# Optimization experiments

Hardware: AMD Instinct MI355X
Metric: run time of the kernel (lower is better)

## Reference

```python
import jax, jax.numpy as jnp
import numpy as np
import math

SQRT2 = float(np.sqrt(2.0))
INV_SQRT_2PI = float(1.0 / np.sqrt(2.0 * np.pi))


def _trunc_prob(x, mu, sigma):
    # Faithful port of TruncNormal.prob with a=-10, b=10
    a, b = -10.0, 10.0
    phi_b = 0.5 * (1.0 + jax.scipy.special.erf((b - mu) / sigma / SQRT2))
    phi_a = 0.5 * (1.0 + jax.scipy.special.erf((a - mu) / sigma / SQRT2))
    xs = jnp.where(x > b, x + 100.0, x)
    xs = jnp.where(xs < a, xs - 100.0, xs)
    xn = (xs - mu) / sigma
    dens = jnp.exp(-0.5 * xn * xn) * INV_SQRT_2PI
    dens = jnp.where((xn > b) | (xn < a), 0.0, dens)
    return dens / (phi_b - phi_a) + 1e-10


def _S_single(zg, tt, Wx, bx, Wt, bt, Wt2, bt2, Wf, bf, Wo, bo):
    # One tiny MLP applied to one group-slice zg (shape [g]) at scalar time tt.
    g = Wx.shape[0]
    x = jnp.tanh(Wx @ zg + bx)
    half = g // 2
    freqs = jnp.exp(jnp.arange(half, dtype=zg.dtype) * (-math.log(10000.0) / half))
    te = tt * freqs
    temb = jnp.concatenate([jnp.sin(te), jnp.cos(te)])  # [g]
    tv = jax.nn.gelu(Wt @ temb + bt, approximate=False)  # torch nn.GELU (exact)
    tv = Wt2 @ tv + bt2
    h = jnp.tanh(Wf @ (x + tv) + bf)
    return jnp.tanh(Wo @ h + bo)[0]  # scalar S


def _derivs(zg, tt, Wx, bx, Wt, bt, Wt2, bt2, Wf, bf, Wo, bo):
    p = (Wx, bx, Wt, bt, Wt2, bt2, Wf, bf, Wo, bo)
    f = lambda z_, t_: _S_single(z_, t_, *p)
    S = f(zg, tt)
    s_z = jax.grad(f, 0)(zg, tt)                    # dS/dz         [g]
    H = jax.jacfwd(jax.grad(f, 0), 0)(zg, tt)       # H[j,k]=d2S/dzj dzk  [g,g]
    dSdt = jax.grad(f, 1)(zg, tt)                   # dS/dt scalar
    return S, s_z, H, dSdt


def reference(z, time_step, mu, sigma, Wx, bx, Wt, bt, Wt2, bt2, Wf, bf, Wo, bo, beta):
    G, g = Wx.shape[0], Wx.shape[1]
    B = z.shape[0]
    tt = time_step[0]

    sig2 = sigma ** 2 + 1e-5
    nlp = -(z - mu) / sig2                                   # nabla_log_phi [B,n_in]
    dlp = -1.0 / sig2                                        # delta_log_phi (scalar-ish)
    dpp = ((z - mu) ** 2 - sigma ** 2) / (sigma ** 4 + 1e-5)  # delta_phi_over_phi
    rho = _trunc_prob(z, mu, sigma)

    to_g = lambda a: a.reshape(B, G, g).transpose(1, 0, 2)   # [G,B,g]
    zr, nlp_r, dpp_r, rho_r = to_g(z), to_g(nlp), to_g(dpp), to_g(rho)

    over_b = jax.vmap(_derivs, in_axes=(0, None) + (None,) * 10)
    over_g = jax.vmap(over_b, in_axes=(0, None) + (0,) * 10)
    S, s_z, H, dSdt = over_g(zr, tt, Wx, bx, Wt, bt, Wt2, bt2, Wf, bf, Wo, bo)
    # S [G,B], s_z [G,B,g], H [G,B,g,g], dSdt [G,B]

    bb = beta.reshape(G, 1, 1)
    u = S[..., None] - bb * jnp.log(jnp.prod(rho_r, axis=2, keepdims=True))  # [G,B,1]
    u_z = s_z - bb * nlp_r                                                    # [G,B,g]
    # torch grad(S.sum(), t): t is a single shared (1,1) tensor -> gradient sums over batch
    dSdt_sum = dSdt.sum(axis=1).reshape(G, 1, 1)
    # grad((rho*u_z).sum(), z_temp): rho and nabla_log_phi are constants wrt z_temp,
    # so gradient = sum_j rho_j * H[j,k]
    corr = jnp.einsum('gbj,gbjk->gbk', rho_r, H)
    u_t = dSdt_sum + bb * corr / (rho_r + 1e-5)
    # grad(s_z.sum(), z_temp)[k] = sum_j H[j,k]
    u_zz = H.sum(axis=2) - bb * dlp
    pde = u_t + 0.5 * u_z ** 2 + 0.125 * bb ** 2 * (nlp_r ** 2 - 2.0 * dpp_r)

    to_bn = lambda a: a.transpose(1, 0, 2).reshape(B, -1)
    return to_bn(pde), to_bn(u_z), u[:, :, 0].transpose(1, 0), to_bn(u_zz)


def setup_inputs() -> dict:
    B, N_IN, g = 8192, 512, 4
    G = N_IN // g
    key = jax.random.key(0)
    ks = jax.random.split(key, 16)

    def lin_w(k, fo, fi):
        return (jax.random.normal(k, (G, fo, fi), jnp.float32) / np.sqrt(fi)).astype(jnp.float32)

    def lin_b(k, fo):
        return (0.01 * jax.random.normal(k, (G, fo), jnp.float32)).astype(jnp.float32)

    return {
        "z": jax.random.normal(ks[0], (B, N_IN), jnp.float32),
        "time_step": jnp.ones((1,), jnp.float32),
        "mu": jnp.zeros((1,), jnp.float32),
        "sigma": jnp.ones((1,), jnp.float32),
        "Wx": lin_w(ks[1], g, g), "bx": lin_b(ks[2], g),
        "Wt": lin_w(ks[3], g, g), "bt": lin_b(ks[4], g),
        "Wt2": lin_w(ks[5], g, g), "bt2": lin_b(ks[6], g),
        "Wf": lin_w(ks[7], g, g), "bf": lin_b(ks[8], g),
        "Wo": lin_w(ks[9], 1, g), "bo": lin_b(ks[10], 1),
        "beta": jnp.ones((G, 1), jnp.float32),
    }
```

## Files before the change

### kernel.cpp

```cpp
#include <hip/hip_runtime.h>
#include <math.h>

#define NG 128
#define NIN 512
#define OFF1 4194304
#define OFF2 8388608
#define OFF3 9437184

#define INV_SQRT_2PI 0.3989422804014327f
#define INV_SQRT2    0.7071067811865476f

__device__ __forceinline__ float ftanh(float x){
    float e = __expf(2.0f*x);
    float r = __builtin_amdgcn_rcpf(e + 1.0f);
    return 1.0f - 2.0f*r;
}
__device__ __forceinline__ float frcp(float x){ return __builtin_amdgcn_rcpf(x); }

__device__ __forceinline__ float gelu_f(float x){
    return 0.5f*x*(1.0f + erff(x*INV_SQRT2));
}
__device__ __forceinline__ float gelu_df(float x){
    return 0.5f*(1.0f + erff(x*INV_SQRT2)) + x*INV_SQRT_2PI*__expf(-0.5f*x*x);
}

__global__ __launch_bounds__(256) void k_fused(const float* __restrict__ z,
    const float* __restrict__ ts,
    const float* __restrict__ mup, const float* __restrict__ sigp,
    const float* __restrict__ Wx, const float* __restrict__ bx,
    const float* __restrict__ Wt, const float* __restrict__ bt,
    const float* __restrict__ Wt2, const float* __restrict__ bt2,
    const float* __restrict__ Wf, const float* __restrict__ bf,
    const float* __restrict__ Wo, const float* __restrict__ bo,
    const float* __restrict__ betap,
    float* __restrict__ partial, float* __restrict__ out){
    const int tid  = threadIdx.x;
    const int gidx = tid & 127;
    const int lb   = tid >> 7;

    const float mu = mup[0], sigma = sigp[0];
    const float sig2     = sigma*sigma + 1e-5f;
    const float inv_sig2 = frcp(sig2);
    const float dlp      = -inv_sig2;
    const float inv_s4   = frcp(sigma*sigma*sigma*sigma + 1e-5f);
    const float inv_sig  = frcp(sigma);
    const float phi_b    = 0.5f*(1.0f+erff((10.0f-mu)*inv_sig*INV_SQRT2));
    const float phi_a    = 0.5f*(1.0f+erff((-10.0f-mu)*inv_sig*INV_SQRT2));
    const float invZ     = frcp(phi_b-phi_a);

    float wx[16], wf[16];
    #pragma unroll
    for (int i=0;i<4;i++){
        float4 a4 = ((const float4*)(Wx + gidx*16))[i];
        wx[i*4+0]=a4.x; wx[i*4+1]=a4.y; wx[i*4+2]=a4.z; wx[i*4+3]=a4.w;
        float4 b4 = ((const float4*)(Wf + gidx*16))[i];
        wf[i*4+0]=b4.x; wf[i*4+1]=b4.y; wf[i*4+2]=b4.z; wf[i*4+3]=b4.w;
    }
    float4 t4;
    t4 = ((const float4*)bx)[gidx];    float bxA[4]={t4.x,t4.y,t4.z,t4.w};
    t4 = ((const float4*)bf)[gidx];    float bfA[4]={t4.x,t4.y,t4.z,t4.w};
    t4 = ((const float4*)Wo)[gidx];    float w3[4] ={t4.x,t4.y,t4.z,t4.w};
    const float bo0 = bo[gidx];
    const float bb  = betap[gidx];

    float tvA[4], dtvA[4];
    {
        const float t  = ts[0];
        const float f1 = 0.01f;
        float te0 = t, te1 = t*f1;
        float s0, c0, s1, c1;
        __sincosf(te0, &s0, &c0);
        __sincosf(te1, &s1, &c1);
        float temb[4]  = { s0, s1, c0, c1 };
        float dtemb[4] = { c0, f1*c1, -s0, -f1*s1 };
        float tg[4], dg[4];
        #pragma unroll
        for (int i=0;i<4;i++){
            float a = bt[gidx*4+i], d = 0.0f;
            #pragma unroll
            for (int j=0;j<4;j++){
                float w = Wt[gidx*16+i*4+j];
                a += w*temb[j]; d += w*dtemb[j];
            }
            tg[i] = gelu_f(a);
            dg[i] = gelu_df(a)*d;
        }
        #pragma unroll
        for (int j=0;j<4;j++){
            float a = bt2[gidx*4+j], d = 0.0f;
            #pragma unroll
            for (int i=0;i<4;i++){
                float w = Wt2[gidx*16+j*4+i];
                a += w*tg[i]; d += w*dg[i];
            }
            tvA[j]  = a;
            dtvA[j] = d;
        }
    }

    float dsdt_acc = 0.0f;
    const int b_base = blockIdx.x*4 + lb*2;

    for (int r=0;r<2;r++){
        const int b = b_base + r;
        float4 zv = *((const float4*)(z + b*NIN + gidx*4));
        float zz[4]={zv.x,zv.y,zv.z,zv.w};

        float x[4], xp[4], u1[4];
        #pragma unroll
        for (int i=0;i<4;i++){
            float a = bxA[i] + wx[i*4]*zz[0]+wx[i*4+1]*zz[1]+wx[i*4+2]*zz[2]+wx[i*4+3]*zz[3];
            x[i] = ftanh(a); xp[i] = 1.0f - x[i]*x[i];
            u1[i] = x[i] + tvA[i];
        }
        float h[4], hp[4];
        float a3 = bo0;
        #pragma unroll
        for (int i=0;i<4;i++){
            float a = bfA[i] + wf[i*4]*u1[0]+wf[i*4+1]*u1[1]+wf[i*4+2]*u1[2]+wf[i*4+3]*u1[3];
            h[i] = ftanh(a); hp[i] = 1.0f - h[i]*h[i];
            a3 += w3[i]*h[i];
        }
        float S = ftanh(a3), sp = 1.0f - S*S;

        float Bm[16];
        #pragma unroll
        for (int i=0;i<4;i++){
            #pragma unroll
            for (int n=0;n<4;n++){
                float s = 0.0f;
                #pragma unroll
                for (int k=0;k<4;k++) s += wf[i*4+k]*xp[k]*wx[k*4+n];
                Bm[i*4+n]=s;
            }
        }
        float w3hp[4], v[4];
        #pragma unroll
        for (int i=0;i<4;i++){ w3hp[i]=w3[i]*hp[i]; v[i]=sp*w3hp[i]; }
        float q[4]={0.f,0.f,0.f,0.f};
        #pragma unroll
        for (int i=0;i<4;i++){
            #pragma unroll
            for (int j=0;j<4;j++) q[j] += v[i]*wf[i*4+j];
        }
        dsdt_acc += q[0]*dtvA[0]+q[1]*dtvA[1]+q[2]*dtvA[2]+q[3]*dtvA[3];

        float c[4];
        #pragma unroll
        for (int n=0;n<4;n++){
            float s=0.0f;
            #pragma unroll
            for (int i=0;i<4;i++) s += w3hp[i]*Bm[i*4+n];
            c[n]=s;
        }
        const float alpha = -2.0f*S*sp;
        float bet[4], gam[4];
        #pragma unroll
        for (int i=0;i<4;i++){ bet[i] = -2.0f*h[i]*v[i]; gam[i] = -2.0f*x[i]*xp[i]*q[i]; }

        float rho[4], nlp[4], dpp[4];
        #pragma unroll
        for (int j=0;j<4;j++){
            float zj = zz[j];
            float xs = zj > 10.0f ? zj+100.0f : zj;
            xs = xs < -10.0f ? xs-100.0f : xs;
            float xn = (xs-mu)*inv_sig;
            float dens = __expf(-0.5f*xn*xn)*INV_SQRT_2PI;
            dens = (xn > 10.0f || xn < -10.0f) ? 0.0f : dens;
            rho[j] = dens*invZ + 1e-10f;
            nlp[j] = -(zj-mu)*inv_sig2;
            float d = zj-mu;
            dpp[j] = (d*d - sigma*sigma)*inv_s4;
        }
        float u_val = S - bb*__logf(rho[0]*rho[1]*rho[2]*rho[3]);

        float rc=0.0f, scs=0.0f;
        #pragma unroll
        for (int j=0;j<4;j++){ rc += rho[j]*c[j]; scs += c[j]; }
        float rB[4], sB[4], rA[4], sA[4];
        #pragma unroll
        for (int i=0;i<4;i++){
            float r1=0.0f, s=0.0f, r2=0.0f, s2=0.0f;
            #pragma unroll
            for (int j=0;j<4;j++){
                r1 += rho[j]*Bm[i*4+j]; s  += Bm[i*4+j];
                r2 += rho[j]*wx[i*4+j]; s2 += wx[i*4+j];
            }
            rB[i]=r1; sB[i]=s; rA[i]=r2; sA[i]=s2;
        }

        float pde[4], uz[4], uzz[4];
        #pragma unroll
        for (int k=0;k<4;k++){
            float corr = alpha*rc*c[k];
            float hsum = alpha*scs*c[k];
            #pragma unroll
            for (int i=0;i<4;i++){
                corr += bet[i]*rB[i]*Bm[i*4+k];
                hsum += bet[i]*sB[i]*Bm[i*4+k];
                corr += gam[i]*rA[i]*wx[i*4+k];
                hsum += gam[i]*sA[i]*wx[i*4+k];
            }
            float uzk = sp*c[k] - bb*nlp[k];
            uz[k]  = uzk;
            uzz[k] = hsum - bb*dlp;
            pde[k] = bb*corr*frcp(rho[k]+1e-5f)
                   + 0.5f*uzk*uzk + 0.125f*bb*bb*(nlp[k]*nlp[k] - 2.0f*dpp[k]);
        }

        const int base = b*NIN + gidx*4;
        *((float4*)(out + base))        = make_float4(pde[0],pde[1],pde[2],pde[3]);
        *((float4*)(out + OFF1 + base)) = make_float4(uz[0],uz[1],uz[2],uz[3]);
        out[OFF2 + b*NG + gidx] = u_val;
        *((float4*)(out + OFF3 + base)) = make_float4(uzz[0],uzz[1],uzz[2],uzz[3]);
    }

    __shared__ float sred[256];
    sred[tid] = dsdt_acc;
    __syncthreads();
    if (tid < 128) partial[blockIdx.x*128 + tid] = sred[tid] + sred[tid+128];
}

__global__ __launch_bounds__(256) void k_red(const float* __restrict__ partial,
                                             float* __restrict__ dsum){
    int g = blockIdx.x;
    int tid = threadIdx.x;
    float a = 0.0f;
    for (int i=tid;i<2048;i+=256) a += partial[i*128+g];
    __shared__ float s[256];
    s[tid] = a;
    __syncthreads();
    if (tid < 64){
        a = s[tid] + s[tid+64] + s[tid+128] + s[tid+192];
        #pragma unroll
        for (int o=32;o>0;o>>=1) a += __shfl_down(a, o);
        if (tid==0) dsum[g] = a;
    }
}

__global__ __launch_bounds__(256) void k_fix(const float* __restrict__ dsum,
                                             float* __restrict__ out){
    const int idx = blockIdx.x*256 + threadIdx.x;
    const float ds = dsum[threadIdx.x & 127];
    float4* p = ((float4*)out) + idx;
    float4 v = *p;
    v.x += ds; v.y += ds; v.z += ds; v.w += ds;
    *p = v;
}

extern "C" void kernel_launch(void* const* d_in, const int* in_sizes, int n_in,
                              void* d_out, int out_size, void* d_ws, size_t ws_size,
                              hipStream_t stream){
    (void)in_sizes; (void)n_in; (void)out_size; (void)ws_size;
    const float* z     = (const float*)d_in[0];
    const float* ts    = (const float*)d_in[1];
    const float* mu    = (const float*)d_in[2];
    const float* sigma = (const float*)d_in[3];
    const float* Wx    = (const float*)d_in[4];
    const float* bx    = (const float*)d_in[5];
    const float* Wt    = (const float*)d_in[6];
    const float* bt    = (const float*)d_in[7];
    const float* Wt2   = (const float*)d_in[8];
    const float* bt2   = (const float*)d_in[9];
    const float* Wf    = (const float*)d_in[10];
    const float* bf    = (const float*)d_in[11];
    const float* Wo    = (const float*)d_in[12];
    const float* bo    = (const float*)d_in[13];
    const float* beta  = (const float*)d_in[14];
    float* out = (float*)d_out;

    float* ws      = (float*)d_ws;
    float* dsum    = ws;
    float* partial = ws + 128;

    k_fused<<<2048,256, 0, stream>>>(z, ts, mu, sigma, Wx, bx, Wt, bt, Wt2, bt2,
                                     Wf, bf, Wo, bo, beta, partial, out);
    k_red  <<<128, 256, 0, stream>>>(partial, dsum);
    k_fix  <<<4096,256, 0, stream>>>(dsum, out);
}
```

Measured before the change: 138.3 us.

## Hoist time-embedding MLP into pre-kernel, one row per thread, nontemporal stores

Moves the per-group time-embedding MLP (sin/cos, GELU, erf) and the scalar sigma constants into a tiny single-block pre-kernel, so the main kernel reads them from workspace instead of recomputing them in every block. The main kernel now handles one batch row per thread with twice as many blocks, and the reduction is widened to match. Outputs that are not re-read use nontemporal stores. The cost is an extra kernel launch and a doubled partial-sum buffer.

```diff
diff --git a/kernel.cpp b/kernel.cpp
--- a/kernel.cpp
+++ b/kernel.cpp
@@ -10,6 +10,8 @@
 #define INV_SQRT_2PI 0.3989422804014327f
 #define INV_SQRT2    0.7071067811865476f
 
+typedef float f32x4 __attribute__((ext_vector_type(4)));
+
 __device__ __forceinline__ float ftanh(float x){
     float e = __expf(2.0f*x);
     float r = __builtin_amdgcn_rcpf(e + 1.0f);
@@ -24,29 +26,78 @@
     return 0.5f*(1.0f + erff(x*INV_SQRT2)) + x*INV_SQRT_2PI*__expf(-0.5f*x*x);
 }
 
-__global__ __launch_bounds__(256) void k_fused(const float* __restrict__ z,
-    const float* __restrict__ ts,
-    const float* __restrict__ mup, const float* __restrict__ sigp,
+__global__ void k_pre(const float* __restrict__ ts,
+                      const float* __restrict__ mup, const float* __restrict__ sigp,
+                      const float* __restrict__ Wt,  const float* __restrict__ bt,
+                      const float* __restrict__ Wt2, const float* __restrict__ bt2,
+                      float* __restrict__ tv_ws, float* __restrict__ dtv_ws,
+                      float* __restrict__ consts){
+    int g = threadIdx.x;
+    if (g == 0){
+        float mu = mup[0], sigma = sigp[0];
+        float sig2   = sigma*sigma + 1e-5f;
+        float phi_b  = 0.5f*(1.0f+erff((10.0f-mu)/sigma*INV_SQRT2));
+        float phi_a  = 0.5f*(1.0f+erff((-10.0f-mu)/sigma*INV_SQRT2));
+        consts[0] = sig2;
+        consts[1] = -1.0f/sig2;
+        consts[2] = 1.0f/(sigma*sigma*sigma*sigma + 1e-5f);
+        consts[3] = 1.0f/(phi_b-phi_a);
+        consts[4] = mu;
+        consts[5] = 1.0f/sigma;
+        consts[6] = sigma;
+    }
+    if (g >= NG) return;
+    float t  = ts[0];
+    const float f1 = 0.01f;
+    float s0, c0, s1, c1;
+    __sincosf(t, &s0, &c0);
+    __sincosf(t*f1, &s1, &c1);
+    float temb[4]  = { s0, s1, c0, c1 };
+    float dtemb[4] = { c0, f1*c1, -s0, -f1*s1 };
+    float tg[4], dg[4];
+    #pragma unroll
+    for (int i=0;i<4;i++){
+        float a = bt[g*4+i], d = 0.0f;
+        #pragma unroll
+        for (int j=0;j<4;j++){
+            float w = Wt[g*16+i*4+j];
+            a += w*temb[j]; d += w*dtemb[j];
+        }
+        tg[i] = gelu_f(a);
+        dg[i] = gelu_df(a)*d;
+    }
+    #pragma unroll
+    for (int j=0;j<4;j++){
+        float a = bt2[g*4+j], d = 0.0f;
+        #pragma unroll
+        for (int i=0;i<4;i++){
+            float w = Wt2[g*16+j*4+i];
+            a += w*tg[i]; d += w*dg[i];
+        }
+        tv_ws[g*4+j]  = a;
+        dtv_ws[g*4+j] = d;
+    }
+}
+
+__global__ __launch_bounds__(256) void k_main(const float* __restrict__ z,
     const float* __restrict__ Wx, const float* __restrict__ bx,
-    const float* __restrict__ Wt, const float* __restrict__ bt,
-    const float* __restrict__ Wt2, const float* __restrict__ bt2,
     const float* __restrict__ Wf, const float* __restrict__ bf,
     const float* __restrict__ Wo, const float* __restrict__ bo,
-    const float* __restrict__ betap,
+    const float* __restrict__ betap, const float* __restrict__ tv_ws,
+    const float* __restrict__ dtv_ws, const float* __restrict__ consts,
     float* __restrict__ partial, float* __restrict__ out){
     const int tid  = threadIdx.x;
     const int gidx = tid & 127;
-    const int lb   = tid >> 7;
-
-    const float mu = mup[0], sigma = sigp[0];
-    const float sig2     = sigma*sigma + 1e-5f;
+    const int b    = blockIdx.x*2 + (tid>>7);
+
+    const float sig2    = consts[0];
+    const float dlp     = consts[1];
+    const float inv_s4  = consts[2];
+    const float invZ    = consts[3];
+    const float mu      = consts[4];
+    const float inv_sig = consts[5];
+    const float sigma   = consts[6];
     const float inv_sig2 = frcp(sig2);
-    const float dlp      = -inv_sig2;
-    const float inv_s4   = frcp(sigma*sigma*sigma*sigma + 1e-5f);
-    const float inv_sig  = frcp(sigma);
-    const float phi_b    = 0.5f*(1.0f+erff((10.0f-mu)*inv_sig*INV_SQRT2));
-    const float phi_a    = 0.5f*(1.0f+erff((-10.0f-mu)*inv_sig*INV_SQRT2));
-    const float invZ     = frcp(phi_b-phi_a);
 
     float wx[16], wf[16];
     #pragma unroll
@@ -57,163 +108,126 @@
         wf[i*4+0]=b4.x; wf[i*4+1]=b4.y; wf[i*4+2]=b4.z; wf[i*4+3]=b4.w;
     }
     float4 t4;
-    t4 = ((const float4*)bx)[gidx];    float bxA[4]={t4.x,t4.y,t4.z,t4.w};
-    t4 = ((const float4*)bf)[gidx];    float bfA[4]={t4.x,t4.y,t4.z,t4.w};
-    t4 = ((const float4*)Wo)[gidx];    float w3[4] ={t4.x,t4.y,t4.z,t4.w};
+    t4 = ((const float4*)bx)[gidx];     float bxA[4]={t4.x,t4.y,t4.z,t4.w};
+    t4 = ((const float4*)bf)[gidx];     float bfA[4]={t4.x,t4.y,t4.z,t4.w};
+    t4 = ((const float4*)Wo)[gidx];     float w3[4] ={t4.x,t4.y,t4.z,t4.w};
+    t4 = ((const float4*)tv_ws)[gidx];  float tvA[4]={t4.x,t4.y,t4.z,t4.w};
+    t4 = ((const float4*)dtv_ws)[gidx]; float dtvA[4]={t4.x,t4.y,t4.z,t4.w};
     const float bo0 = bo[gidx];
     const float bb  = betap[gidx];
 
-    float tvA[4], dtvA[4];
-    {
-        const float t  = ts[0];
-        const float f1 = 0.01f;
-        float te0 = t, te1 = t*f1;
-        float s0, c0, s1, c1;
-        __sincosf(te0, &s0, &c0);
-        __sincosf(te1, &s1, &c1);
-        float temb[4]  = { s0, s1, c0, c1 };
-        float dtemb[4] = { c0, f1*c1, -s0, -f1*s1 };
-        float tg[4], dg[4];
+    float4 zv = *((const float4*)(z + b*NIN + gidx*4));
+    float zz[4]={zv.x,zv.y,zv.z,zv.w};
+
+    float x[4], xp[4], u1[4];
+    #pragma unroll
+    for (int i=0;i<4;i++){
+        float a = bxA[i] + wx[i*4]*zz[0]+wx[i*4+1]*zz[1]+wx[i*4+2]*zz[2]+wx[i*4+3]*zz[3];
+        x[i] = ftanh(a); xp[i] = 1.0f - x[i]*x[i];
+        u1[i] = x[i] + tvA[i];
+    }
+    float h[4], hp[4];
+    float a3 = bo0;
+    #pragma unroll
+    for (int i=0;i<4;i++){
+        float a = bfA[i] + wf[i*4]*u1[0]+wf[i*4+1]*u1[1]+wf[i*4+2]*u1[2]+wf[i*4+3]*u1[3];
+        h[i] = ftanh(a); hp[i] = 1.0f - h[i]*h[i];
+        a3 += w3[i]*h[i];
+    }
+    float S = ftanh(a3), sp = 1.0f - S*S;
+
+    float Bm[16];
+    #pragma unroll
+    for (int i=0;i<4;i++){
+        #pragma unroll
+        for (int n=0;n<4;n++){
+            float s = 0.0f;
+            #pragma unroll
+            for (int k=0;k<4;k++) s += wf[i*4+k]*xp[k]*wx[k*4+n];
+            Bm[i*4+n]=s;
+        }
+    }
+    float w3hp[4], v[4];
+    #pragma unroll
+    for (int i=0;i<4;i++){ w3hp[i]=w3[i]*hp[i]; v[i]=sp*w3hp[i]; }
+    float q[4]={0.f,0.f,0.f,0.f};
+    #pragma unroll
+    for (int i=0;i<4;i++){
+        #pragma unroll
+        for (int j=0;j<4;j++) q[j] += v[i]*wf[i*4+j];
+    }
+    float dsdt_acc = q[0]*dtvA[0]+q[1]*dtvA[1]+q[2]*dtvA[2]+q[3]*dtvA[3];
+
+    float c[4];
+    #pragma unroll
+    for (int n=0;n<4;n++){
+        float s=0.0f;
+        #pragma unroll
+        for (int i=0;i<4;i++) s += w3hp[i]*Bm[i*4+n];
+        c[n]=s;
+    }
+    const float alpha = -2.0f*S*sp;
+    float bet[4], gam[4];
+    #pragma unroll
+    for (int i=0;i<4;i++){ bet[i] = -2.0f*h[i]*v[i]; gam[i] = -2.0f*x[i]*xp[i]*q[i]; }
+
+    float rho[4], nlp[4], dpp[4];
+    #pragma unroll
+    for (int j=0;j<4;j++){
+        float zj = zz[j];
+        float xs = zj > 10.0f ? zj+100.0f : zj;
+        xs = xs < -10.0f ? xs-100.0f : xs;
+        float xn = (xs-mu)*inv_sig;
+        float dens = __expf(-0.5f*xn*xn)*INV_SQRT_2PI;
+        dens = (xn > 10.0f || xn < -10.0f) ? 0.0f : dens;
+        rho[j] = dens*invZ + 1e-10f;
+        nlp[j] = -(zj-mu)*inv_sig2;
+        float d = zj-mu;
+        dpp[j] = (d*d - sigma*sigma)*inv_s4;
+    }
+    float u_val = S - bb*__logf(rho[0]*rho[1]*rho[2]*rho[3]);
+
+    float rc=0.0f, scs=0.0f;
+    #pragma unroll
+    for (int j=0;j<4;j++){ rc += rho[j]*c[j]; scs += c[j]; }
+    float rB[4], sB[4], rA[4], sA[4];
+    #pragma unroll
+    for (int i=0;i<4;i++){
+        float r1=0.0f, s=0.0f, r2=0.0f, s2=0.0f;
+        #pragma unroll
+        for (int j=0;j<4;j++){
+            r1 += rho[j]*Bm[i*4+j]; s  += Bm[i*4+j];
+            r2 += rho[j]*wx[i*4+j]; s2 += wx[i*4+j];
+        }
+        rB[i]=r1; sB[i]=s; rA[i]=r2; sA[i]=s2;
+    }
+
+    float pde[4], uz[4], uzz[4];
+    #pragma unroll
+    for (int k=0;k<4;k++){
+        float corr = alpha*rc*c[k];
+        float hsum = alpha*scs*c[k];
         #pragma unroll
         for (int i=0;i<4;i++){
-            float a = bt[gidx*4+i], d = 0.0f;
-            #pragma unroll
-            for (int j=0;j<4;j++){
-                float w = Wt[gidx*16+i*4+j];
-                a += w*temb[j]; d += w*dtemb[j];
-            }
-            tg[i] = gelu_f(a);
-            dg[i] = gelu_df(a)*d;
-        }
-        #pragma unroll
-        for (int j=0;j<4;j++){
-            float a = bt2[gidx*4+j], d = 0.0f;
-            #pragma unroll
-            for (int i=0;i<4;i++){
-                float w = Wt2[gidx*16+j*4+i];
-                a += w*tg[i]; d += w*dg[i];
-            }
-            tvA[j]  = a;
-            dtvA[j] = d;
-        }
-    }
-
-    float dsdt_acc = 0.0f;
-    const int b_base = blockIdx.x*4 + lb*2;
-
-    for (int r=0;r<2;r++){
-        const int b = b_base + r;
-        float4 zv = *((const float4*)(z + b*NIN + gidx*4));
-        float zz[4]={zv.x,zv.y,zv.z,zv.w};
-
-        float x[4], xp[4], u1[4];
-        #pragma unroll
-        for (int i=0;i<4;i++){
-            float a = bxA[i] + wx[i*4]*zz[0]+wx[i*4+1]*zz[1]+wx[i*4+2]*zz[2]+wx[i*4+3]*zz[3];
-            x[i] = ftanh(a); xp[i] = 1.0f - x[i]*x[i];
-            u1[i] = x[i] + tvA[i];
-        }
-        float h[4], hp[4];
-        float a3 = bo0;
-        #pragma unroll
-        for (int i=0;i<4;i++){
-            float a = bfA[i] + wf[i*4]*u1[0]+wf[i*4+1]*u1[1]+wf[i*4+2]*u1[2]+wf[i*4+3]*u1[3];
-            h[i] = ftanh(a); hp[i] = 1.0f - h[i]*h[i];
-            a3 += w3[i]*h[i];
-        }
-        float S = ftanh(a3), sp = 1.0f - S*S;
-
-        float Bm[16];
-        #pragma unroll
-        for (int i=0;i<4;i++){
-            #pragma unroll
-            for (int n=0;n<4;n++){
-                float s = 0.0f;
-                #pragma unroll
-                for (int k=0;k<4;k++) s += wf[i*4+k]*xp[k]*wx[k*4+n];
-                Bm[i*4+n]=s;
-            }
-        }
-        float w3hp[4], v[4];
-        #pragma unroll
-        for (int i=0;i<4;i++){ w3hp[i]=w3[i]*hp[i]; v[i]=sp*w3hp[i]; }
-        float q[4]={0.f,0.f,0.f,0.f};
-        #pragma unroll
-        for (int i=0;i<4;i++){
-            #pragma unroll
-            for (int j=0;j<4;j++) q[j] += v[i]*wf[i*4+j];
-        }
-        dsdt_acc += q[0]*dtvA[0]+q[1]*dtvA[1]+q[2]*dtvA[2]+q[3]*dtvA[3];
-
-        float c[4];
-        #pragma unroll
-        for (int n=0;n<4;n++){
-            float s=0.0f;
-            #pragma unroll
-            for (int i=0;i<4;i++) s += w3hp[i]*Bm[i*4+n];
-            c[n]=s;
-        }
-        const float alpha = -2.0f*S*sp;
-        float bet[4], gam[4];
-        #pragma unroll
-        for (int i=0;i<4;i++){ bet[i] = -2.0f*h[i]*v[i]; gam[i] = -2.0f*x[i]*xp[i]*q[i]; }
-
-        float rho[4], nlp[4], dpp[4];
-        #pragma unroll
-        for (int j=0;j<4;j++){
-            float zj = zz[j];
-            float xs = zj > 10.0f ? zj+100.0f : zj;
-            xs = xs < -10.0f ? xs-100.0f : xs;
-            float xn = (xs-mu)*inv_sig;
-            float dens = __expf(-0.5f*xn*xn)*INV_SQRT_2PI;
-            dens = (xn > 10.0f || xn < -10.0f) ? 0.0f : dens;
-            rho[j] = dens*invZ + 1e-10f;
-            nlp[j] = -(zj-mu)*inv_sig2;
-            float d = zj-mu;
-            dpp[j] = (d*d - sigma*sigma)*inv_s4;
-        }
-        float u_val = S - bb*__logf(rho[0]*rho[1]*rho[2]*rho[3]);
-
-        float rc=0.0f, scs=0.0f;
-        #pragma unroll
-        for (int j=0;j<4;j++){ rc += rho[j]*c[j]; scs += c[j]; }
-        float rB[4], sB[4], rA[4], sA[4];
-        #pragma unroll
-        for (int i=0;i<4;i++){
-            float r1=0.0f, s=0.0f, r2=0.0f, s2=0.0f;
-            #pragma unroll
-            for (int j=0;j<4;j++){
-                r1 += rho[j]*Bm[i*4+j]; s  += Bm[i*4+j];
-                r2 += rho[j]*wx[i*4+j]; s2 += wx[i*4+j];
-            }
-            rB[i]=r1; sB[i]=s; rA[i]=r2; sA[i]=s2;
-        }
-
-        float pde[4], uz[4], uzz[4];
-        #pragma unroll
-        for (int k=0;k<4;k++){
-            float corr = alpha*rc*c[k];
-            float hsum = alpha*scs*c[k];
-            #pragma unroll
-            for (int i=0;i<4;i++){
-                corr += bet[i]*rB[i]*Bm[i*4+k];
-                hsum += bet[i]*sB[i]*Bm[i*4+k];
-                corr += gam[i]*rA[i]*wx[i*4+k];
-                hsum += gam[i]*sA[i]*wx[i*4+k];
-            }
-            float uzk = sp*c[k] - bb*nlp[k];
-            uz[k]  = uzk;
-            uzz[k] = hsum - bb*dlp;
-            pde[k] = bb*corr*frcp(rho[k]+1e-5f)
-                   + 0.5f*uzk*uzk + 0.125f*bb*bb*(nlp[k]*nlp[k] - 2.0f*dpp[k]);
-        }
-
-        const int base = b*NIN + gidx*4;
-        *((float4*)(out + base))        = make_float4(pde[0],pde[1],pde[2],pde[3]);
-        *((float4*)(out + OFF1 + base)) = make_float4(uz[0],uz[1],uz[2],uz[3]);
-        out[OFF2 + b*NG + gidx] = u_val;
-        *((float4*)(out + OFF3 + base)) = make_float4(uzz[0],uzz[1],uzz[2],uzz[3]);
-    }
+            corr += bet[i]*rB[i]*Bm[i*4+k];
+            hsum += bet[i]*sB[i]*Bm[i*4+k];
+            corr += gam[i]*rA[i]*wx[i*4+k];
+            hsum += gam[i]*sA[i]*wx[i*4+k];
+        }
+        float uzk = sp*c[k] - bb*nlp[k];
+        uz[k]  = uzk;
+        uzz[k] = hsum - bb*dlp;
+        pde[k] = bb*corr*frcp(rho[k]+1e-5f)
+               + 0.5f*uzk*uzk + 0.125f*bb*bb*(nlp[k]*nlp[k] - 2.0f*dpp[k]);
+    }
+
+    const int base = b*NIN + gidx*4;
+    *((float4*)(out + base)) = make_float4(pde[0],pde[1],pde[2],pde[3]);
+    f32x4 uzv  = { uz[0],  uz[1],  uz[2],  uz[3]  };
+    f32x4 uzzv = { uzz[0], uzz[1], uzz[2], uzz[3] };
+    __builtin_nontemporal_store(uzv,  (f32x4*)(out + OFF1 + base));
+    __builtin_nontemporal_store(u_val, out + OFF2 + b*NG + gidx);
+    __builtin_nontemporal_store(uzzv, (f32x4*)(out + OFF3 + base));
 
     __shared__ float sred[256];
     sred[tid] = dsdt_acc;
@@ -226,7 +240,7 @@
     int g = blockIdx.x;
     int tid = threadIdx.x;
     float a = 0.0f;
-    for (int i=tid;i<2048;i+=256) a += partial[i*128+g];
+    for (int i=tid;i<4096;i+=256) a += partial[i*128+g];
     __shared__ float s[256];
     s[tid] = a;
     __syncthreads();
@@ -270,11 +284,15 @@
     float* out = (float*)d_out;
 
     float* ws      = (float*)d_ws;
-    float* dsum    = ws;
-    float* partial = ws + 128;
-
-    k_fused<<<2048,256, 0, stream>>>(z, ts, mu, sigma, Wx, bx, Wt, bt, Wt2, bt2,
-                                     Wf, bf, Wo, bo, beta, partial, out);
-    k_red  <<<128, 256, 0, stream>>>(partial, dsum);
-    k_fix  <<<4096,256, 0, stream>>>(dsum, out);
-}
+    float* tv_ws   = ws;
+    float* dtv_ws  = ws + 512;
+    float* consts  = ws + 1024;
+    float* dsum    = ws + 1032;
+    float* partial = ws + 1160;
+
+    k_pre <<<1,   128, 0, stream>>>(ts, mu, sigma, Wt, bt, Wt2, bt2, tv_ws, dtv_ws, consts);
+    k_main<<<4096,256, 0, stream>>>(z, Wx, bx, Wf, bf, Wo, bo, beta, tv_ws, dtv_ws,
+                                    consts, partial, out);
+    k_red <<<128, 256, 0, stream>>>(partial, dsum);
+    k_fix <<<4096,256, 0, stream>>>(dsum, out);
+}
```

Measured after the change: 129.5 us. -6.4%, faster.
